# Kernel optimization log

Hardware: AMD Instinct MI355X
Metric: run time of the kernel (lower is better)

## Reference

```python
import jax, jax.numpy as jnp
import numpy as np

N_EMBED = 2048
N_HEAD = 16
HEAD_SIZE = N_EMBED // N_HEAD  # 128


def rotate_half(x):
    x1, x2 = jnp.split(x, 2, axis=-1)
    return jnp.concatenate((-x2, x1), axis=-1)


def setup_inputs() -> dict:
    key = jax.random.key(0)
    k_x, k_qkv, k_proj, k_b = jax.random.split(key, 4)
    B, T = 4, 2048
    x = jax.random.normal(k_x, (B, T, N_EMBED), dtype=jnp.float32)
    # weights stored as [in, out] so y = x @ W (equivalent param'n of nn.Linear)
    w_qkv = jax.random.normal(k_qkv, (N_EMBED, 3 * N_EMBED), dtype=jnp.float32) * (N_EMBED ** -0.5)
    w_proj = jax.random.normal(k_proj, (N_EMBED, N_EMBED), dtype=jnp.float32) * (N_EMBED ** -0.5)
    b_proj = jax.random.normal(k_b, (N_EMBED,), dtype=jnp.float32) * 0.02
    return {"x": x, "w_qkv": w_qkv, "w_proj": w_proj, "b_proj": b_proj}


def reference(x, w_qkv, w_proj, b_proj):
    B, T, C = x.shape
    H, D = N_HEAD, HEAD_SIZE
    qkv = x @ w_qkv                                   # [B,T,3C]
    q, k, v = jnp.split(qkv, 3, axis=2)
    q = q.reshape(B, T, H, D).transpose(0, 2, 1, 3)   # [B,H,T,D]
    k = k.reshape(B, T, H, D).transpose(0, 2, 1, 3)
    v = v.reshape(B, T, H, D).transpose(0, 2, 1, 3)
    # RoPE in fp32
    inv_freq = 1.0 / (10000.0 ** (jnp.arange(0, D, 2, dtype=jnp.float32) / D))
    t = jnp.arange(T, dtype=jnp.float32)
    freqs = jnp.einsum('i,j->ij', t, inv_freq)        # [T,D/2]
    emb = jnp.concatenate((freqs, freqs), axis=-1)    # [T,D]
    cos = jnp.cos(emb)[None, None, :, :]
    sin = jnp.sin(emb)[None, None, :, :]
    qf = q.astype(jnp.float32)
    kf = k.astype(jnp.float32)
    q = (qf * cos + rotate_half(qf) * sin).astype(v.dtype)
    k = (kf * cos + rotate_half(kf) * sin).astype(v.dtype)
    # causal SDPA
    scale = 1.0 / jnp.sqrt(jnp.asarray(D, dtype=q.dtype))
    scores = jnp.einsum('bhqd,bhkd->bhqk', q, k) * scale
    causal = jnp.tril(jnp.ones((T, T), dtype=bool))
    scores = jnp.where(causal[None, None, :, :], scores, jnp.finfo(scores.dtype).min)
    attn = jax.nn.softmax(scores, axis=-1)
    out = jnp.einsum('bhqk,bhkd->bhqd', attn, v)      # [B,H,T,D]
    out = out.transpose(0, 2, 1, 3).reshape(B, T, C)
    return out @ w_proj + b_proj
```

## Files before the change

### kernel.cpp

```cpp
#include <hip/hip_runtime.h>
#include <hip/hip_bf16.h>
#include <cstdint>
#include <cstddef>

typedef __bf16 bf16x8 __attribute__((ext_vector_type(8)));
typedef __bf16 bf16x4 __attribute__((ext_vector_type(4)));
typedef float  f32x4  __attribute__((ext_vector_type(4)));

__device__ __forceinline__ void lds_load16(const void* gsrc, void* ldst) {
    __builtin_amdgcn_global_load_lds(
        (const __attribute__((address_space(1))) unsigned int*)gsrc,
        (__attribute__((address_space(3))) unsigned int*)ldst,
        16, 0, 0);
}

__global__ __launch_bounds__(256) void cvt_k(const float* __restrict__ in,
                                             __bf16* __restrict__ out, int n8) {
    int i = blockIdx.x * 256 + threadIdx.x;
    if (i >= n8) return;
    const float4* p4 = (const float4*)in + (size_t)i * 2;
    float4 a = p4[0], b = p4[1];
    bf16x8 o;
    o[0] = (__bf16)a.x; o[1] = (__bf16)a.y; o[2] = (__bf16)a.z; o[3] = (__bf16)a.w;
    o[4] = (__bf16)b.x; o[5] = (__bf16)b.y; o[6] = (__bf16)b.z; o[7] = (__bf16)b.w;
    *((bf16x8*)out + i) = o;
}

__global__ __launch_bounds__(256) void transp_k(const float* __restrict__ W,
                                                __bf16* __restrict__ WT, int R, int C) {
    __shared__ float tile[32][33];
    int tx = threadIdx.x & 31, ty = threadIdx.x >> 5;
    int c0 = blockIdx.x * 32, r0 = blockIdx.y * 32;
#pragma unroll
    for (int k = 0; k < 4; ++k)
        tile[ty + 8 * k][tx] = W[(size_t)(r0 + ty + 8 * k) * C + c0 + tx];
    __syncthreads();
#pragma unroll
    for (int k = 0; k < 4; ++k)
        WT[(size_t)(c0 + ty + 8 * k) * R + r0 + tx] = (__bf16)tile[tx][ty + 8 * k];
}

__global__ __launch_bounds__(256) void sincos_k(float2* __restrict__ sc) {
    int idx = blockIdx.x * 256 + threadIdx.x;
    int t = idx >> 6, j = idx & 63;
    float inv = powf(10000.f, -(float)j / 64.f);
    float f = (float)t * inv;
    float s, c;
    sincosf(f, &s, &c);
    sc[idx] = make_float2(c, s);
}

__global__ __launch_bounds__(256) void rope_k(__bf16* __restrict__ qb, __bf16* __restrict__ kb,
                                              const float2* __restrict__ sc) {
    unsigned idx = blockIdx.x * 256 + threadIdx.x;
    int tensor = idx >> 20;
    unsigned i = idx & 0xFFFFFu;
    int jb = (i & 7) * 8;
    int t = (i >> 3) & 2047;
    int bh = i >> 14;
    __bf16* p = tensor ? kb : qb;
    size_t base = ((size_t)bh * 2048 + t) * 128;
    bf16x8 lo = *(bf16x8*)(p + base + jb);
    bf16x8 hi = *(bf16x8*)(p + base + 64 + jb);
    const float2* s2 = sc + t * 64 + jb;
    float scale = tensor ? 1.f : 0.08838834764831845f;
    bf16x8 olo, ohi;
#pragma unroll
    for (int e = 0; e < 8; ++e) {
        float c = s2[e].x, s = s2[e].y;
        float x1 = (float)lo[e], x2 = (float)hi[e];
        olo[e] = (__bf16)((x1 * c - x2 * s) * scale);
        ohi[e] = (__bf16)((x2 * c + x1 * s) * scale);
    }
    *(bf16x8*)(p + base + jb) = olo;
    *(bf16x8*)(p + base + 64 + jb) = ohi;
}

__global__ __launch_bounds__(512, 2) void gemm8_k(const __bf16* __restrict__ A,
                                                  const __bf16* __restrict__ Bt,
                                                  int nbn, int mode,
                                                  __bf16* __restrict__ qb, __bf16* __restrict__ kb,
                                                  __bf16* __restrict__ vt,
                                                  float* __restrict__ outp,
                                                  const float* __restrict__ bias) {
    __shared__ __bf16 lds[2][2][2][128 * 64];
    const int K = 2048, NT = K / 64;
    int nwg = gridDim.x;
    int per = nwg >> 3;
    int bid = blockIdx.x;
    int wg = (bid & 7) * per + (bid >> 3);
    int bm = wg / nbn, bn = wg % nbn;
    int m0 = bm * 256, n0 = bn * 256;
    int tid = threadIdx.x;
    int lane = tid & 63, wave = tid >> 6;
    int wm = wave >> 2, wn = wave & 3;
    int lr = lane & 15, lg = lane >> 4;

    f32x4 acc[8][4] = {};

    auto stageA = [&](int db, int sub, int kt) {
#pragma unroll
        for (int l = 0; l < 2; ++l) {
            int chunk = l * 512 + tid;
            int r = chunk >> 3, c16 = chunk & 7;
            int rg = m0 + ((r >> 6) << 7) + (sub << 6) + (r & 63);
            lds_load16(A + (size_t)rg * K + (kt << 6) + ((c16 ^ (r & 7)) << 3),
                       &lds[db][0][sub][chunk * 8]);
        }
    };
    auto stageB = [&](int db, int sub, int kt) {
#pragma unroll
        for (int l = 0; l < 2; ++l) {
            int chunk = l * 512 + tid;
            int r = chunk >> 3, c16 = chunk & 7;
            int rg = n0 + ((r >> 5) << 6) + (sub << 5) + (r & 31);
            lds_load16(Bt + (size_t)rg * K + (kt << 6) + ((c16 ^ (r & 7)) << 3),
                       &lds[db][1][sub][chunk * 8]);
        }
    };
    auto rdA = [&](int db, int sub, int q, int kk) -> bf16x8 {
        int r = (wm << 6) + (q << 4) + lr;
        int cb = ((kk << 6) + (lg << 4)) ^ ((r & 7) << 4);
        return *(const bf16x8*)((const char*)&lds[db][0][sub][0] + r * 128 + cb);
    };
    auto rdB = [&](int db, int j, int kk) -> bf16x8 {
        int sub = j >> 1;
        int r = (wn << 5) + ((j & 1) << 4) + lr;
        int cb = ((kk << 6) + (lg << 4)) ^ ((r & 7) << 4);
        return *(const bf16x8*)((const char*)&lds[db][1][sub][0] + r * 128 + cb);
    };

    stageA(0, 0, 0); stageB(0, 0, 0); stageB(0, 1, 0); stageA(0, 1, 0);
    asm volatile("s_waitcnt vmcnt(0)" ::: "memory");
    __builtin_amdgcn_s_barrier();

    bf16x8 a[4], a2[4], b[4], b2[4];
    for (int t = 0; t < NT; ++t) {
        int db = t & 1, dn = db ^ 1;
        bool pf = (t + 1 < NT);
#pragma unroll
        for (int q = 0; q < 4; ++q) a[q] = rdA(db, 0, q, 0);
#pragma unroll
        for (int j = 0; j < 4; ++j) b[j] = rdB(db, j, 0);
        if (pf) { stageA(dn, 0, t + 1); stageB(dn, 0, t + 1); }
        __builtin_amdgcn_s_barrier();
        __builtin_amdgcn_s_setprio(1);
#pragma unroll
        for (int q = 0; q < 4; ++q)
#pragma unroll
            for (int j = 0; j < 4; ++j)
                acc[q][j] = __builtin_amdgcn_mfma_f32_16x16x32_bf16(a[q], b[j], acc[q][j], 0, 0, 0);
        __builtin_amdgcn_s_setprio(0);
#pragma unroll
        for (int q = 0; q < 4; ++q) a2[q] = rdA(db, 0, q, 1);
#pragma unroll
        for (int j = 0; j < 4; ++j) b2[j] = rdB(db, j, 1);
        if (pf) {
            stageB(dn, 1, t + 1);
            asm volatile("s_waitcnt vmcnt(6)" ::: "memory");
        } else {
            asm volatile("s_waitcnt vmcnt(0)" ::: "memory");
        }
        __builtin_amdgcn_s_barrier();
        __builtin_amdgcn_s_setprio(1);
#pragma unroll
        for (int q = 0; q < 4; ++q)
#pragma unroll
            for (int j = 0; j < 4; ++j)
                acc[q][j] = __builtin_amdgcn_mfma_f32_16x16x32_bf16(a2[q], b2[j], acc[q][j], 0, 0, 0);
        __builtin_amdgcn_s_setprio(0);
#pragma unroll
        for (int q = 0; q < 4; ++q) a[q] = rdA(db, 1, q, 0);
#pragma unroll
        for (int q = 0; q < 4; ++q) a2[q] = rdA(db, 1, q, 1);
        if (pf) stageA(dn, 1, t + 1);
        __builtin_amdgcn_s_barrier();
        __builtin_amdgcn_s_setprio(1);
#pragma unroll
        for (int q = 0; q < 4; ++q)
#pragma unroll
            for (int j = 0; j < 4; ++j)
                acc[q + 4][j] = __builtin_amdgcn_mfma_f32_16x16x32_bf16(a[q], b[j], acc[q + 4][j], 0, 0, 0);
        __builtin_amdgcn_s_setprio(0);
        asm volatile("s_waitcnt lgkmcnt(0)" ::: "memory");
        if (pf) asm volatile("s_waitcnt vmcnt(2)" ::: "memory");
        __builtin_amdgcn_s_barrier();
        __builtin_amdgcn_s_setprio(1);
#pragma unroll
        for (int q = 0; q < 4; ++q)
#pragma unroll
            for (int j = 0; j < 4; ++j)
                acc[q + 4][j] = __builtin_amdgcn_mfma_f32_16x16x32_bf16(a2[q], b2[j], acc[q + 4][j], 0, 0, 0);
        __builtin_amdgcn_s_setprio(0);
    }

    if (mode == 0) {
#pragma unroll
        for (int q = 0; q < 8; ++q) {
            int row_t = (wm << 7) + ((q >> 2) << 6) + ((q & 3) << 4) + (lg << 2);
#pragma unroll
            for (int j = 0; j < 4; ++j) {
                int c = n0 + (wn << 6) + (j << 4) + lr;
                int which = c >> 11;
                int h = (c & 2047) >> 7;
                int d = c & 127;
#pragma unroll
                for (int r = 0; r < 4; ++r) {
                    int row = m0 + row_t + r;
                    int b_ = row >> 11, tt = row & 2047;
                    __bf16 val = (__bf16)acc[q][j][r];
                    size_t bh = (size_t)(b_ * 16 + h);
                    if (which == 0)      qb[(bh * 2048 + tt) * 128 + d] = val;
                    else if (which == 1) kb[(bh * 2048 + tt) * 128 + d] = val;
                    else                 vt[(bh * 128 + d) * 2048 + tt] = val;
                }
            }
        }
    } else {
#pragma unroll
        for (int q = 0; q < 8; ++q) {
            int row_t = (wm << 7) + ((q >> 2) << 6) + ((q & 3) << 4) + (lg << 2);
#pragma unroll
            for (int j = 0; j < 4; ++j) {
                int col = n0 + (wn << 6) + (j << 4) + lr;
                float bv = bias[col];
#pragma unroll
                for (int r = 0; r < 4; ++r) {
                    int row = m0 + row_t + r;
                    outp[(size_t)row * 2048 + col] = acc[q][j][r] + bv;
                }
            }
        }
    }
}

__global__ __launch_bounds__(256, 2) void attn_k(const __bf16* __restrict__ qb,
                                                 const __bf16* __restrict__ kb,
                                                 const __bf16* __restrict__ vt,
                                                 __bf16* __restrict__ ao) {
    __shared__ __bf16 Ks[64 * 128];
    __shared__ __bf16 Vs[128 * 64];
    __shared__ __bf16 Ps[4][16 * 64];

    int bid = blockIdx.x;
    int qt = 31 - (bid >> 6);
    int bh = bid & 63;
    int qs = qt * 64;
    int tid = threadIdx.x, wave = tid >> 6, lane = tid & 63;
    int lr = lane & 15, lg = lane >> 4;

    bf16x8 qf[4];
    const __bf16* Qrow = qb + ((size_t)bh * 2048 + qs + wave * 16 + lr) * 128;
#pragma unroll
    for (int kk = 0; kk < 4; ++kk) qf[kk] = *(const bf16x8*)(Qrow + kk * 32 + lg * 8);

    f32x4 ot[8] = {};
    float m_run = -1e30f, l_run = 0.f;

    for (int ks = 0; ks <= qs; ks += 64) {
#pragma unroll
        for (int i = 0; i < 4; ++i) {
            int c = tid + i * 256;
            {
                int row = c >> 4;
                int cc = c ^ (row & 7);
                int dd = (cc & 15) * 8;
                lds_load16(kb + ((size_t)bh * 2048 + ks + row) * 128 + dd, Ks + c * 8);
            }
            {
                int row = c >> 3;
                int cc = c ^ (row & 7);
                int tt = (cc & 7) * 8;
                lds_load16(vt + ((size_t)bh * 128 + row) * 2048 + ks + tt, Vs + c * 8);
            }
        }
        __syncthreads();

        f32x4 st[4];
        __builtin_amdgcn_s_setprio(1);
#pragma unroll
        for (int mt = 0; mt < 4; ++mt) {
            f32x4 s = {};
#pragma unroll
            for (int kk = 0; kk < 4; ++kk) {
                int row = mt * 16 + lr;
                const __bf16* kp = Ks + row * 128 + ((((kk * 64 + lg * 16)) ^ ((row & 7) << 4)) >> 1);
                bf16x8 afr = *(const bf16x8*)kp;
                s = __builtin_amdgcn_mfma_f32_16x16x32_bf16(afr, qf[kk], s, 0, 0, 0);
            }
            st[mt] = s;
        }
        __builtin_amdgcn_s_setprio(0);

        if (ks == qs) {
            int q = qs + wave * 16 + lr;
#pragma unroll
            for (int mt = 0; mt < 4; ++mt)
#pragma unroll
                for (int r = 0; r < 4; ++r) {
                    int kv = ks + mt * 16 + lg * 4 + r;
                    if (kv > q) st[mt][r] = -1e30f;
                }
        }

        float pm = -1e30f;
#pragma unroll
        for (int mt = 0; mt < 4; ++mt)
#pragma unroll
            for (int r = 0; r < 4; ++r) pm = fmaxf(pm, st[mt][r]);
        pm = fmaxf(pm, __shfl_xor(pm, 16));
        pm = fmaxf(pm, __shfl_xor(pm, 32));
        float nm = fmaxf(m_run, pm);
        float alpha = __expf(m_run - nm);
        float psum = 0.f;
#pragma unroll
        for (int mt = 0; mt < 4; ++mt)
#pragma unroll
            for (int r = 0; r < 4; ++r) {
                float p = __expf(st[mt][r] - nm);
                psum += p;
                st[mt][r] = p;
            }
        psum += __shfl_xor(psum, 16);
        psum += __shfl_xor(psum, 32);
        l_run = l_run * alpha + psum;
        m_run = nm;
#pragma unroll
        for (int t8 = 0; t8 < 8; ++t8) ot[t8] *= alpha;

#pragma unroll
        for (int mt = 0; mt < 4; ++mt) {
            bf16x4 pk;
#pragma unroll
            for (int r = 0; r < 4; ++r) pk[r] = (__bf16)st[mt][r];
            int byteoff = lr * 128 + (((mt * 32 + lg * 8)) ^ ((lr & 7) << 4));
            *(bf16x4*)((char*)&Ps[wave][0] + byteoff) = pk;
        }

        bf16x8 pfr[2];
#pragma unroll
        for (int kk = 0; kk < 2; ++kk) {
            const char* pp = (const char*)&Ps[wave][0] + lr * 128 + (((kk * 64 + lg * 16)) ^ ((lr & 7) << 4));
            pfr[kk] = *(const bf16x8*)pp;
        }
        __builtin_amdgcn_s_setprio(1);
#pragma unroll
        for (int dt = 0; dt < 8; ++dt) {
#pragma unroll
            for (int kk = 0; kk < 2; ++kk) {
                int row = dt * 16 + lr;
                const __bf16* vp = Vs + row * 64 + ((((kk * 64 + lg * 16)) ^ ((row & 7) << 4)) >> 1);
                bf16x8 afr = *(const bf16x8*)vp;
                ot[dt] = __builtin_amdgcn_mfma_f32_16x16x32_bf16(afr, pfr[kk], ot[dt], 0, 0, 0);
            }
        }
        __builtin_amdgcn_s_setprio(0);
        __syncthreads();
    }

    float inv = 1.f / l_run;
    int b_ = bh >> 4, h = bh & 15;
    size_t rowbase = ((size_t)b_ * 2048 + qs + wave * 16 + lr) * 2048 + h * 128;
#pragma unroll
    for (int dt = 0; dt < 8; ++dt) {
        bf16x4 o;
#pragma unroll
        for (int r = 0; r < 4; ++r) o[r] = (__bf16)(ot[dt][r] * inv);
        *(bf16x4*)(ao + rowbase + dt * 16 + lg * 4) = o;
    }
}

extern "C" void kernel_launch(void* const* d_in, const int* in_sizes, int n_in,
                              void* d_out, int out_size, void* d_ws, size_t ws_size,
                              hipStream_t stream) {
    const float* x      = (const float*)d_in[0];
    const float* w_qkv  = (const float*)d_in[1];
    const float* w_proj = (const float*)d_in[2];
    const float* b_proj = (const float*)d_in[3];
    float* out = (float*)d_out;
    char* ws = (char*)d_ws;

    __bf16* xb  = (__bf16*)(ws);
    __bf16* wqt = (__bf16*)(ws + 33554432);
    __bf16* wpt = (__bf16*)(ws + 58720256);
    __bf16* qb  = (__bf16*)(ws + 67108864);
    __bf16* kb  = (__bf16*)(ws + 100663296);
    __bf16* vt  = (__bf16*)(ws + 134217728);
    __bf16* ao  = (__bf16*)(ws + 167772160);
    float2* sc  = (float2*)(ws + 201326592);

    hipLaunchKernelGGL(cvt_k, dim3(8192), dim3(256), 0, stream, x, xb, 2097152);
    hipLaunchKernelGGL(transp_k, dim3(192, 64), dim3(256), 0, stream, w_qkv, wqt, 2048, 6144);
    hipLaunchKernelGGL(transp_k, dim3(64, 64), dim3(256), 0, stream, w_proj, wpt, 2048, 2048);
    hipLaunchKernelGGL(sincos_k, dim3(512), dim3(256), 0, stream, sc);
    hipLaunchKernelGGL(gemm8_k, dim3(768), dim3(512), 0, stream,
                       xb, wqt, 24, 0, qb, kb, vt, (float*)nullptr, (const float*)nullptr);
    hipLaunchKernelGGL(rope_k, dim3(8192), dim3(256), 0, stream, qb, kb, sc);
    hipLaunchKernelGGL(attn_k, dim3(2048), dim3(256), 0, stream, qb, kb, vt, ao);
    hipLaunchKernelGGL(gemm8_k, dim3(256), dim3(512), 0, stream,
                       ao, wpt, 8, 1, (__bf16*)nullptr, (__bf16*)nullptr, (__bf16*)nullptr,
                       out, b_proj);
}
```

Before: 435.8 us.

## Software-pipeline LDS fragment reads one phase ahead of MFMA in GEMM loop

Restructures the GEMM main loop so that the LDS fragment reads for the next MFMA phase are issued before the current phase's MFMAs, with a prologue that preloads the first fragments. It also loosens the initial vmcnt wait and adds sched_barriers so the compiler keeps this interleaving. The aim is to hide LDS read latency behind matrix-core work. In exchange it adds register pressure from the extra live fragments and depends on vmcnt counts being exactly right, which risks reading stale LDS data.

After: 438.7 us. No clear change (+0.7%).

```diff
diff --git a/kernel.cpp b/kernel.cpp
--- a/kernel.cpp
+++ b/kernel.cpp
@@ -131,67 +131,75 @@
     };
 
     stageA(0, 0, 0); stageB(0, 0, 0); stageB(0, 1, 0); stageA(0, 1, 0);
-    asm volatile("s_waitcnt vmcnt(0)" ::: "memory");
+    asm volatile("s_waitcnt vmcnt(2)" ::: "memory");
     __builtin_amdgcn_s_barrier();
 
-    bf16x8 a[4], a2[4], b[4], b2[4];
+    bf16x8 a0[4], a1[4], b0[4], b1[4];
+#pragma unroll
+    for (int q = 0; q < 4; ++q) a0[q] = rdA(0, 0, q, 0);
+#pragma unroll
+    for (int j = 0; j < 4; ++j) b0[j] = rdB(0, j, 0);
+
     for (int t = 0; t < NT; ++t) {
         int db = t & 1, dn = db ^ 1;
         bool pf = (t + 1 < NT);
 #pragma unroll
-        for (int q = 0; q < 4; ++q) a[q] = rdA(db, 0, q, 0);
-#pragma unroll
-        for (int j = 0; j < 4; ++j) b[j] = rdB(db, j, 0);
+        for (int q = 0; q < 4; ++q) a1[q] = rdA(db, 0, q, 1);
+#pragma unroll
+        for (int j = 0; j < 4; ++j) b1[j] = rdB(db, j, 1);
         if (pf) { stageA(dn, 0, t + 1); stageB(dn, 0, t + 1); }
+        __builtin_amdgcn_sched_barrier(0);
+        __builtin_amdgcn_s_setprio(1);
+#pragma unroll
+        for (int q = 0; q < 4; ++q)
+#pragma unroll
+            for (int j = 0; j < 4; ++j)
+                acc[q][j] = __builtin_amdgcn_mfma_f32_16x16x32_bf16(a0[q], b0[j], acc[q][j], 0, 0, 0);
+        __builtin_amdgcn_s_setprio(0);
+        if (pf) asm volatile("s_waitcnt vmcnt(4)" ::: "memory");
+        else    asm volatile("s_waitcnt vmcnt(0)" ::: "memory");
         __builtin_amdgcn_s_barrier();
+#pragma unroll
+        for (int q = 0; q < 4; ++q) a0[q] = rdA(db, 1, q, 0);
+        if (pf) stageB(dn, 1, t + 1);
+        __builtin_amdgcn_sched_barrier(0);
         __builtin_amdgcn_s_setprio(1);
 #pragma unroll
         for (int q = 0; q < 4; ++q)
 #pragma unroll
             for (int j = 0; j < 4; ++j)
-                acc[q][j] = __builtin_amdgcn_mfma_f32_16x16x32_bf16(a[q], b[j], acc[q][j], 0, 0, 0);
-        __builtin_amdgcn_s_setprio(0);
-#pragma unroll
-        for (int q = 0; q < 4; ++q) a2[q] = rdA(db, 0, q, 1);
-#pragma unroll
-        for (int j = 0; j < 4; ++j) b2[j] = rdB(db, j, 1);
+                acc[q][j] = __builtin_amdgcn_mfma_f32_16x16x32_bf16(a1[q], b1[j], acc[q][j], 0, 0, 0);
+        __builtin_amdgcn_s_setprio(0);
+        __builtin_amdgcn_s_barrier();
+#pragma unroll
+        for (int q = 0; q < 4; ++q) a1[q] = rdA(db, 1, q, 1);
+        if (pf) stageA(dn, 1, t + 1);
+        __builtin_amdgcn_sched_barrier(0);
+        __builtin_amdgcn_s_setprio(1);
+#pragma unroll
+        for (int q = 0; q < 4; ++q)
+#pragma unroll
+            for (int j = 0; j < 4; ++j)
+                acc[q + 4][j] = __builtin_amdgcn_mfma_f32_16x16x32_bf16(a0[q], b0[j], acc[q + 4][j], 0, 0, 0);
+        __builtin_amdgcn_s_setprio(0);
+        if (pf) asm volatile("s_waitcnt vmcnt(2)" ::: "memory");
+        else    asm volatile("s_waitcnt vmcnt(0)" ::: "memory");
+        __builtin_amdgcn_s_barrier();
         if (pf) {
-            stageB(dn, 1, t + 1);
-            asm volatile("s_waitcnt vmcnt(6)" ::: "memory");
-        } else {
-            asm volatile("s_waitcnt vmcnt(0)" ::: "memory");
-        }
+#pragma unroll
+            for (int q = 0; q < 4; ++q) a0[q] = rdA(dn, 0, q, 0);
+#pragma unroll
+            for (int j = 0; j < 4; ++j) b0[j] = rdB(dn, j, 0);
+        }
+        __builtin_amdgcn_sched_barrier(0);
+        __builtin_amdgcn_s_setprio(1);
+#pragma unroll
+        for (int q = 0; q < 4; ++q)
+#pragma unroll
+            for (int j = 0; j < 4; ++j)
+                acc[q + 4][j] = __builtin_amdgcn_mfma_f32_16x16x32_bf16(a1[q], b1[j], acc[q + 4][j], 0, 0, 0);
+        __builtin_amdgcn_s_setprio(0);
         __builtin_amdgcn_s_barrier();
-        __builtin_amdgcn_s_setprio(1);
-#pragma unroll
-        for (int q = 0; q < 4; ++q)
-#pragma unroll
-            for (int j = 0; j < 4; ++j)
-                acc[q][j] = __builtin_amdgcn_mfma_f32_16x16x32_bf16(a2[q], b2[j], acc[q][j], 0, 0, 0);
-        __builtin_amdgcn_s_setprio(0);
-#pragma unroll
-        for (int q = 0; q < 4; ++q) a[q] = rdA(db, 1, q, 0);
-#pragma unroll
-        for (int q = 0; q < 4; ++q) a2[q] = rdA(db, 1, q, 1);
-        if (pf) stageA(dn, 1, t + 1);
-        __builtin_amdgcn_s_barrier();
-        __builtin_amdgcn_s_setprio(1);
-#pragma unroll
-        for (int q = 0; q < 4; ++q)
-#pragma unroll
-            for (int j = 0; j < 4; ++j)
-                acc[q + 4][j] = __builtin_amdgcn_mfma_f32_16x16x32_bf16(a[q], b[j], acc[q + 4][j], 0, 0, 0);
-        __builtin_amdgcn_s_setprio(0);
-        asm volatile("s_waitcnt lgkmcnt(0)" ::: "memory");
-        if (pf) asm volatile("s_waitcnt vmcnt(2)" ::: "memory");
-        __builtin_amdgcn_s_barrier();
-        __builtin_amdgcn_s_setprio(1);
-#pragma unroll
-        for (int q = 0; q < 4; ++q)
-#pragma unroll
-            for (int j = 0; j < 4; ++j)
-                acc[q + 4][j] = __builtin_amdgcn_mfma_f32_16x16x32_bf16(a2[q], b2[j], acc[q + 4][j], 0, 0, 0);
-        __builtin_amdgcn_s_setprio(0);
     }
 
     if (mode == 0) {
```
